# Kernel optimization log

Hardware: AMD Instinct MI355X
Metric: run time of the kernel (lower is better)

The kernel has to match this reference:

```python
import jax, jax.numpy as jnp
import numpy as np

DIM = 1024
H = 16
DH = DIM // H
THETA = 10000.0


def _rotary_cos_sin(dtype):
    # Faithful to original: rotary is called on q with shape (B, H, 1, DH) and
    # seq_dim=1, so "positions" are t = arange(num_heads).
    inv_freq = 1.0 / (THETA ** (jnp.arange(0, DH, 2, dtype=jnp.float32) / DH))
    t = jnp.arange(H, dtype=jnp.float32)
    freqs = t[:, None] * inv_freq[None, :]          # (H, DH/2)
    emb = jnp.concatenate([freqs, freqs], axis=-1)   # (H, DH)
    cos = jnp.cos(emb)[None, :, None, :].astype(dtype)  # (1, H, 1, DH)
    sin = jnp.sin(emb)[None, :, None, :].astype(dtype)
    return cos, sin


def _rotate_half(x):
    x1, x2 = x[..., : DH // 2], x[..., DH // 2 :]
    return jnp.concatenate([-x2, x1], axis=-1)


def setup_inputs() -> dict:
    key = jax.random.key(0)
    ks = jax.random.split(key, 6)
    B, N = 16, 4096
    s = 1.0 / np.sqrt(DIM)
    return {
        "x": jax.random.normal(ks[0], (B, N, DIM), dtype=jnp.float32),
        "Wq": jax.random.normal(ks[1], (DIM, DIM), dtype=jnp.float32) * s,
        "Wk": jax.random.normal(ks[2], (DIM, DIM), dtype=jnp.float32) * s,
        "Wv": jax.random.normal(ks[3], (DIM, DIM), dtype=jnp.float32) * s,
        "Wp": jax.random.normal(ks[4], (DIM, DIM), dtype=jnp.float32) * s,
        "bp": jax.random.normal(ks[5], (DIM,), dtype=jnp.float32) * 0.01,
    }


def reference(x, Wq, Wk, Wv, Wp, bp):
    B, N, C = x.shape
    scale = DH ** -0.5
    # projections (weights stored as (in, out); x @ W)
    q = (x[:, :1, :] @ Wq).reshape(B, 1, H, DH).transpose(0, 2, 1, 3)  # (B,H,1,DH)
    k = (x @ Wk).reshape(B, N, H, DH).transpose(0, 2, 1, 3)            # (B,H,N,DH)
    v = (x @ Wv).reshape(B, N, H, DH).transpose(0, 2, 1, 3)            # (B,H,N,DH)
    cos, sin = _rotary_cos_sin(x.dtype)
    q = q * cos + _rotate_half(q) * sin
    k = k * cos + _rotate_half(k) * sin  # broadcasts over N (per original)
    attn = jnp.einsum("bhqd,bhkd->bhqk", q, k) * scale  # (B,H,1,N)
    attn = jax.nn.softmax(attn, axis=-1)
    out = jnp.einsum("bhqk,bhkd->bhqd", attn, v)        # (B,H,1,DH)
    out = out.transpose(0, 2, 1, 3).reshape(B, 1, C)
    return out @ Wp + bp
```

## Files before the change

### kernel.cpp

```cpp
#include <hip/hip_runtime.h>

#define NB 16
#define SEQ 4096
#define DIMC 1024
#define NH 16
#define DH 64
#define NC 64
#define RS 32

#define OFF_Q    0
#define OFF_WTIL 16384
#define OFF_PMAX 278528
#define OFF_LC   294912
#define OFF_E    311296
#define OFF_YOUT 1359872
#define OFF_HO   9748480

__global__ __launch_bounds__(256) void kq(const float* __restrict__ x,
                                          const float* __restrict__ Wq,
                                          float* __restrict__ qws) {
  const int jc = blockIdx.x, b = blockIdx.y, t = threadIdx.x;
  const int d = t & 63, g = t >> 6;
  const int j = jc * 64 + d;
  const float* x0 = x + (size_t)b * SEQ * DIMC;
  __shared__ float red[256];
  float a = 0.f;
  #pragma unroll 8
  for (int c = g * 256; c < g * 256 + 256; ++c)
    a = fmaf(x0[c], Wq[(size_t)c * DIMC + j], a);
  red[t] = a;
  __syncthreads();
  if (t < 64)
    qws[b * DIMC + jc * 64 + t] = red[t] + red[64 + t] + red[128 + t] + red[192 + t];
}

__global__ __launch_bounds__(256) void kw(const float* __restrict__ Wk,
                                          const float* __restrict__ qws,
                                          float* __restrict__ wtil) {
  const int cb = blockIdx.x, b = blockIdx.y, t = threadIdx.x;
  const int w = t >> 6, l = t & 63;
  float4 qreg[4];
  {
    const float4* q4 = (const float4*)(qws + b * DIMC + l * 16);
    #pragma unroll
    for (int i = 0; i < 4; ++i) qreg[i] = q4[i];
  }
  const int h = l >> 2;
  float* wt = wtil + ((size_t)b * NH + h) * DIMC;
  #pragma unroll 4
  for (int i = 0; i < 16; ++i) {
    const int c = cb * 64 + w * 16 + i;
    const float4* row = (const float4*)(Wk + (size_t)c * DIMC) + l * 4;
    float s = 0.f;
    #pragma unroll
    for (int k = 0; k < 4; ++k) {
      float4 rv = row[k];
      s = fmaf(rv.x, qreg[k].x, s); s = fmaf(rv.y, qreg[k].y, s);
      s = fmaf(rv.z, qreg[k].z, s); s = fmaf(rv.w, qreg[k].w, s);
    }
    s += __shfl_xor(s, 1);
    s += __shfl_xor(s, 2);
    if ((l & 3) == 0) wt[c] = s * 0.125f;
  }
}

__device__ __forceinline__ float dot16(const float4* xv, const float4* wv) {
  float s = 0.f;
  #pragma unroll
  for (int i = 0; i < 4; ++i) {
    s = fmaf(xv[i].x, wv[i].x, s); s = fmaf(xv[i].y, wv[i].y, s);
    s = fmaf(xv[i].z, wv[i].z, s); s = fmaf(xv[i].w, wv[i].w, s);
  }
  return s;
}

__global__ __launch_bounds__(256) void kS(const float* __restrict__ x,
                                          const float* __restrict__ wtil,
                                          float* __restrict__ e,
                                          float* __restrict__ pmax,
                                          float* __restrict__ Lc) {
  const int nc = blockIdx.x, b = blockIdx.y, t = threadIdx.x;
  const int w = t >> 6, l = t & 63;

  const float4* wt4 = (const float4*)wtil + ((size_t)b * NH + w * 4) * 256;
  float4 wv[4][4];
  #pragma unroll
  for (int h = 0; h < 4; ++h)
    #pragma unroll
    for (int i = 0; i < 4; ++i) wv[h][i] = wt4[h * 256 + i * 64 + l];
  const float4* x4 = (const float4*)x + ((size_t)b * SEQ + nc * 64) * 256;
  float4 va = make_float4(0.f, 0.f, 0.f, 0.f);

  for (int r = 0; r < 64; r += 2) {
    float4 xa[4], xb[4];
    #pragma unroll
    for (int i = 0; i < 4; ++i) xa[i] = x4[r * 256 + i * 64 + l];
    #pragma unroll
    for (int i = 0; i < 4; ++i) xb[i] = x4[(r + 1) * 256 + i * 64 + l];
    float4 sa, sb;
    sa.x = dot16(xa, wv[0]); sa.y = dot16(xa, wv[1]);
    sa.z = dot16(xa, wv[2]); sa.w = dot16(xa, wv[3]);
    sb.x = dot16(xb, wv[0]); sb.y = dot16(xb, wv[1]);
    sb.z = dot16(xb, wv[2]); sb.w = dot16(xb, wv[3]);
    #pragma unroll
    for (int o = 1; o < 64; o <<= 1) {
      sa.x += __shfl_xor(sa.x, o); sa.y += __shfl_xor(sa.y, o);
      sa.z += __shfl_xor(sa.z, o); sa.w += __shfl_xor(sa.w, o);
      sb.x += __shfl_xor(sb.x, o); sb.y += __shfl_xor(sb.y, o);
      sb.z += __shfl_xor(sb.z, o); sb.w += __shfl_xor(sb.w, o);
    }
    if (l == r) va = sa;
    if (l == r + 1) va = sb;
  }

  float4 m4 = va;
  #pragma unroll
  for (int o = 1; o < 64; o <<= 1) {
    m4.x = fmaxf(m4.x, __shfl_xor(m4.x, o)); m4.y = fmaxf(m4.y, __shfl_xor(m4.y, o));
    m4.z = fmaxf(m4.z, __shfl_xor(m4.z, o)); m4.w = fmaxf(m4.w, __shfl_xor(m4.w, o));
  }
  float4 pv;
  pv.x = __expf(va.x - m4.x); pv.y = __expf(va.y - m4.y);
  pv.z = __expf(va.z - m4.z); pv.w = __expf(va.w - m4.w);
  float4 s4 = pv;
  #pragma unroll
  for (int o = 1; o < 64; o <<= 1) {
    s4.x += __shfl_xor(s4.x, o); s4.y += __shfl_xor(s4.y, o);
    s4.z += __shfl_xor(s4.z, o); s4.w += __shfl_xor(s4.w, o);
  }
  ((float4*)e)[((size_t)b * SEQ + nc * 64 + l) * 4 + w] = pv;
  if (l == 0) {
    ((float4*)(pmax + ((size_t)b * NC + nc) * NH))[w] = m4;
    ((float4*)(Lc + ((size_t)b * NC + nc) * NH))[w] = s4;
  }
}

__global__ __launch_bounds__(256) void kY(const float* __restrict__ x,
                                          const float* __restrict__ e,
                                          const float* __restrict__ pmax,
                                          const float* __restrict__ Lc,
                                          float* __restrict__ yout) {
  const int rs = blockIdx.x, b = blockIdx.y, t = threadIdx.x;
  __shared__ float4 sc4[NC][4];
  __shared__ float4 pl[64][4];

  if (t < 64) {
    const int ch = t;
    float scl[16];
    #pragma unroll
    for (int h = 0; h < 16; ++h) {
      float m  = pmax[((size_t)b * NC + ch) * NH + h];
      float lc = Lc[((size_t)b * NC + ch) * NH + h];
      float M = m;
      #pragma unroll
      for (int o = 1; o < 64; o <<= 1) M = fmaxf(M, __shfl_xor(M, o));
      float ex = __expf(m - M);
      float lw = lc * ex;
      #pragma unroll
      for (int o = 1; o < 64; o <<= 1) lw += __shfl_xor(lw, o);
      scl[h] = ex / lw;
    }
    #pragma unroll
    for (int q = 0; q < 4; ++q)
      sc4[ch][q] = make_float4(scl[4 * q], scl[4 * q + 1], scl[4 * q + 2], scl[4 * q + 3]);
  }

  const float4* x4 = (const float4*)x + (size_t)b * SEQ * 256;
  const float4* e4 = (const float4*)e + (size_t)b * SEQ * 4;

  float4 acc[16];
  #pragma unroll
  for (int h = 0; h < 16; ++h) acc[h] = make_float4(0.f, 0.f, 0.f, 0.f);

  for (int c4 = 0; c4 < 2; ++c4) {
    const int ch = rs * 2 + c4;
    __syncthreads();
    {
      const int r = t >> 2, qd = t & 3;
      float4 ev = e4[(size_t)(ch * 64 + r) * 4 + qd];
      float4 s  = sc4[ch][qd];
      pl[r][qd] = make_float4(ev.x * s.x, ev.y * s.y, ev.z * s.z, ev.w * s.w);
    }
    __syncthreads();

    const float4* xc = x4 + (size_t)(ch * 64) * 256;
    for (int r = 0; r < 64; r += 4) {
      float4 xv0 = xc[(size_t)(r + 0) * 256 + t];
      float4 xv1 = xc[(size_t)(r + 1) * 256 + t];
      float4 xv2 = xc[(size_t)(r + 2) * 256 + t];
      float4 xv3 = xc[(size_t)(r + 3) * 256 + t];
      #pragma unroll
      for (int rr = 0; rr < 4; ++rr) {
        float4 xv = (rr == 0) ? xv0 : (rr == 1) ? xv1 : (rr == 2) ? xv2 : xv3;
        float4 p0 = pl[r + rr][0], p1 = pl[r + rr][1];
        float4 p2 = pl[r + rr][2], p3 = pl[r + rr][3];
        #define ACC(h, ev) acc[h].x = fmaf(ev, xv.x, acc[h].x); acc[h].y = fmaf(ev, xv.y, acc[h].y); \
                           acc[h].z = fmaf(ev, xv.z, acc[h].z); acc[h].w = fmaf(ev, xv.w, acc[h].w)
        ACC(0, p0.x); ACC(1, p0.y); ACC(2, p0.z); ACC(3, p0.w);
        ACC(4, p1.x); ACC(5, p1.y); ACC(6, p1.z); ACC(7, p1.w);
        ACC(8, p2.x); ACC(9, p2.y); ACC(10, p2.z); ACC(11, p2.w);
        ACC(12, p3.x); ACC(13, p3.y); ACC(14, p3.z); ACC(15, p3.w);
        #undef ACC
      }
    }
  }

  float4* yo = (float4*)yout + (((size_t)b * RS + rs) * NH) * 256 + t;
  #pragma unroll
  for (int h = 0; h < 16; ++h) yo[h * 256] = acc[h];
}

__global__ __launch_bounds__(256) void kV(const float* __restrict__ yout,
                                          const float* __restrict__ Wv,
                                          float* __restrict__ ho) {
  const int cq = blockIdx.x, h = blockIdx.y, b = blockIdx.z, t = threadIdx.x;
  __shared__ float ysum[DIMC];
  __shared__ float red[256];
  #pragma unroll
  for (int i = 0; i < 4; ++i) {
    const int c = i * 256 + t;
    float s = 0.f;
    #pragma unroll 8
    for (int r = 0; r < RS; ++r)
      s += yout[(((size_t)b * RS + r) * NH + h) * DIMC + c];
    ysum[c] = s;
  }
  __syncthreads();
  const int d = t & 15, g = t >> 4;
  float a = 0.f;
  #pragma unroll 8
  for (int i = 0; i < 64; ++i)
    a = fmaf(ysum[g * 64 + i], Wv[(size_t)(g * 64 + i) * DIMC + h * DH + cq * 16 + d], a);
  red[t] = a;
  __syncthreads();
  if (t < 16) {
    float s = 0.f;
    #pragma unroll
    for (int j = 0; j < 16; ++j) s += red[j * 16 + t];
    ho[(size_t)b * DIMC + h * DH + cq * 16 + t] = s;
  }
}

__global__ __launch_bounds__(256) void k_out(const float* __restrict__ ho,
                                             const float* __restrict__ Wp,
                                             const float* __restrict__ bp,
                                             float* __restrict__ out) {
  const int jc = blockIdx.x, b = blockIdx.y, t = threadIdx.x;
  __shared__ float hs[1024];
  __shared__ float red[256];
  for (int i = t; i < 1024; i += 256)
    hs[i] = ho[(size_t)b * DIMC + i];
  __syncthreads();
  const int d = t & 63, g = t >> 6;
  const int j = jc * 64 + d;
  float a = 0.f;
  #pragma unroll 8
  for (int i = g * 256; i < g * 256 + 256; ++i)
    a = fmaf(hs[i], Wp[(size_t)i * DIMC + j], a);
  red[t] = a;
  __syncthreads();
  if (t < 64)
    out[(size_t)b * DIMC + jc * 64 + t] =
        red[t] + red[64 + t] + red[128 + t] + red[192 + t] + bp[jc * 64 + t];
}

extern "C" void kernel_launch(void* const* d_in, const int* in_sizes, int n_in,
                              void* d_out, int out_size, void* d_ws, size_t ws_size,
                              hipStream_t stream) {
  const float* x  = (const float*)d_in[0];
  const float* Wq = (const float*)d_in[1];
  const float* Wk = (const float*)d_in[2];
  const float* Wv = (const float*)d_in[3];
  const float* Wp = (const float*)d_in[4];
  const float* bp = (const float*)d_in[5];
  float* out = (float*)d_out;
  float* ws = (float*)d_ws;

  float* qws  = ws + OFF_Q;
  float* wtil = ws + OFF_WTIL;
  float* pmax = ws + OFF_PMAX;
  float* Lc   = ws + OFF_LC;
  float* e    = ws + OFF_E;
  float* yout = ws + OFF_YOUT;
  float* ho   = ws + OFF_HO;

  kq<<<dim3(16, NB), 256, 0, stream>>>(x, Wq, qws);
  kw<<<dim3(16, NB), 256, 0, stream>>>(Wk, qws, wtil);
  kS<<<dim3(NC, NB), 256, 0, stream>>>(x, wtil, e, pmax, Lc);
  kY<<<dim3(RS, NB), 256, 0, stream>>>(x, e, pmax, Lc, yout);
  kV<<<dim3(4, NH, NB), 256, 0, stream>>>(yout, Wv, ho);
  k_out<<<dim3(16, NB), 256, 0, stream>>>(ho, Wp, bp, out);
}
```

Before: 527.1 us.

## Compute attention scores with bf16 MFMA instead of FP32 dot products

Rewrites the score kernel so the x·wtil products for 64 rows by 16 heads use the 16x16x32 bf16 MFMA. The folded query weights are converted to bf16 and staged in LDS, and x rows are converted to bf16 in registers. This replaces the per-row FP32 dot products and 64-lane shuffle reductions with matrix-core work and a small LDS reduction for the max and sum. Inputs are rounded to bf16, which loses precision in the logits before the exponential.

```diff
diff --git a/kernel.cpp b/kernel.cpp
--- a/kernel.cpp
+++ b/kernel.cpp
@@ -1,4 +1,5 @@
 #include <hip/hip_runtime.h>
+#include <hip/hip_bf16.h>
 
 #define NB 16
 #define SEQ 4096
@@ -7,6 +8,9 @@
 #define DH 64
 #define NC 64
 #define RS 32
+
+typedef short bf16x8 __attribute__((ext_vector_type(8)));
+typedef float f32x4 __attribute__((ext_vector_type(4)));
 
 #define OFF_Q    0
 #define OFF_WTIL 16384
@@ -64,16 +68,6 @@
   }
 }
 
-__device__ __forceinline__ float dot16(const float4* xv, const float4* wv) {
-  float s = 0.f;
-  #pragma unroll
-  for (int i = 0; i < 4; ++i) {
-    s = fmaf(xv[i].x, wv[i].x, s); s = fmaf(xv[i].y, wv[i].y, s);
-    s = fmaf(xv[i].z, wv[i].z, s); s = fmaf(xv[i].w, wv[i].w, s);
-  }
-  return s;
-}
-
 __global__ __launch_bounds__(256) void kS(const float* __restrict__ x,
                                           const float* __restrict__ wtil,
                                           float* __restrict__ e,
@@ -81,57 +75,63 @@
                                           float* __restrict__ Lc) {
   const int nc = blockIdx.x, b = blockIdx.y, t = threadIdx.x;
   const int w = t >> 6, l = t & 63;
-
-  const float4* wt4 = (const float4*)wtil + ((size_t)b * NH + w * 4) * 256;
-  float4 wv[4][4];
-  #pragma unroll
-  for (int h = 0; h < 4; ++h)
-    #pragma unroll
-    for (int i = 0; i < 4; ++i) wv[h][i] = wt4[h * 256 + i * 64 + l];
-  const float4* x4 = (const float4*)x + ((size_t)b * SEQ + nc * 64) * 256;
-  float4 va = make_float4(0.f, 0.f, 0.f, 0.f);
-
-  for (int r = 0; r < 64; r += 2) {
-    float4 xa[4], xb[4];
-    #pragma unroll
-    for (int i = 0; i < 4; ++i) xa[i] = x4[r * 256 + i * 64 + l];
-    #pragma unroll
-    for (int i = 0; i < 4; ++i) xb[i] = x4[(r + 1) * 256 + i * 64 + l];
-    float4 sa, sb;
-    sa.x = dot16(xa, wv[0]); sa.y = dot16(xa, wv[1]);
-    sa.z = dot16(xa, wv[2]); sa.w = dot16(xa, wv[3]);
-    sb.x = dot16(xb, wv[0]); sb.y = dot16(xb, wv[1]);
-    sb.z = dot16(xb, wv[2]); sb.w = dot16(xb, wv[3]);
-    #pragma unroll
-    for (int o = 1; o < 64; o <<= 1) {
-      sa.x += __shfl_xor(sa.x, o); sa.y += __shfl_xor(sa.y, o);
-      sa.z += __shfl_xor(sa.z, o); sa.w += __shfl_xor(sa.w, o);
-      sb.x += __shfl_xor(sb.x, o); sb.y += __shfl_xor(sb.y, o);
-      sb.z += __shfl_xor(sb.z, o); sb.w += __shfl_xor(sb.w, o);
-    }
-    if (l == r) va = sa;
-    if (l == r + 1) va = sb;
-  }
-
-  float4 m4 = va;
-  #pragma unroll
-  for (int o = 1; o < 64; o <<= 1) {
-    m4.x = fmaxf(m4.x, __shfl_xor(m4.x, o)); m4.y = fmaxf(m4.y, __shfl_xor(m4.y, o));
-    m4.z = fmaxf(m4.z, __shfl_xor(m4.z, o)); m4.w = fmaxf(m4.w, __shfl_xor(m4.w, o));
-  }
-  float4 pv;
-  pv.x = __expf(va.x - m4.x); pv.y = __expf(va.y - m4.y);
-  pv.z = __expf(va.z - m4.z); pv.w = __expf(va.w - m4.w);
-  float4 s4 = pv;
-  #pragma unroll
-  for (int o = 1; o < 64; o <<= 1) {
-    s4.x += __shfl_xor(s4.x, o); s4.y += __shfl_xor(s4.y, o);
-    s4.z += __shfl_xor(s4.z, o); s4.w += __shfl_xor(s4.w, o);
-  }
-  ((float4*)e)[((size_t)b * SEQ + nc * 64 + l) * 4 + w] = pv;
-  if (l == 0) {
-    ((float4*)(pmax + ((size_t)b * NC + nc) * NH))[w] = m4;
-    ((float4*)(Lc + ((size_t)b * NC + nc) * NH))[w] = s4;
+  __shared__ unsigned short wlds[16][1032];
+  __shared__ float wred[4][16];
+
+  const float* wt = wtil + (size_t)b * NH * DIMC;
+  for (int i = t; i < NH * DIMC; i += 256) {
+    __hip_bfloat16 hb = __float2bfloat16(wt[i]);
+    wlds[i >> 10][i & 1023] = *reinterpret_cast<unsigned short*>(&hb);
+  }
+  __syncthreads();
+
+  const int lw = l & 15, lg = l >> 4;
+  const int r0 = nc * 64 + w * 16;
+  const float* xrow = x + ((size_t)b * SEQ + r0 + lw) * DIMC;
+
+  f32x4 acc = {0.f, 0.f, 0.f, 0.f};
+  #pragma unroll 4
+  for (int kk = 0; kk < 32; ++kk) {
+    const int k0 = kk * 32 + lg * 8;
+    float4 a0 = *(const float4*)(xrow + k0);
+    float4 a1 = *(const float4*)(xrow + k0 + 4);
+    union { float4 v; float f[4]; } ua, ub;
+    ua.v = a0; ub.v = a1;
+    bf16x8 af;
+    #pragma unroll
+    for (int j = 0; j < 4; ++j) {
+      __hip_bfloat16 h1 = __float2bfloat16(ua.f[j]);
+      __hip_bfloat16 h2 = __float2bfloat16(ub.f[j]);
+      af[j]     = (short)*reinterpret_cast<unsigned short*>(&h1);
+      af[4 + j] = (short)*reinterpret_cast<unsigned short*>(&h2);
+    }
+    bf16x8 bfr = *(const bf16x8*)(&wlds[lw][k0]);
+    acc = __builtin_amdgcn_mfma_f32_16x16x32_bf16(af, bfr, acc, 0, 0, 0);
+  }
+
+  float m = fmaxf(fmaxf(acc[0], acc[1]), fmaxf(acc[2], acc[3]));
+  m = fmaxf(m, __shfl_xor(m, 16));
+  m = fmaxf(m, __shfl_xor(m, 32));
+  if (l < 16) wred[w][l] = m;
+  __syncthreads();
+  const float mc = fmaxf(fmaxf(wred[0][lw], wred[1][lw]),
+                         fmaxf(wred[2][lw], wred[3][lw]));
+  float p0 = __expf(acc[0] - mc), p1 = __expf(acc[1] - mc);
+  float p2 = __expf(acc[2] - mc), p3 = __expf(acc[3] - mc);
+  float s = (p0 + p1) + (p2 + p3);
+  s += __shfl_xor(s, 16);
+  s += __shfl_xor(s, 32);
+  __syncthreads();
+  if (l < 16) wred[w][l] = s;
+  __syncthreads();
+
+  float* ep = e + ((size_t)b * SEQ + r0 + lg * 4) * NH + lw;
+  ep[0 * NH] = p0; ep[1 * NH] = p1; ep[2 * NH] = p2; ep[3 * NH] = p3;
+
+  if (w == 0 && l < 16) {
+    float Ls = (wred[0][l] + wred[1][l]) + (wred[2][l] + wred[3][l]);
+    pmax[((size_t)b * NC + nc) * NH + l] = mc;
+    Lc  [((size_t)b * NC + nc) * NH + l] = Ls;
   }
 }
 
```

New measurement: 517.5 us. Within noise of the previous version (-1.8%).
